# Kernel optimization log

Measured on AMD Instinct MI355X. Metric: run time of the kernel, lower is better.

Reference implementation:

```python
import jax, jax.numpy as jnp
import numpy as np

DIM = 384
HEADS = 6
HIDDEN = int(DIM * 4.0)
EPS = 1e-6

def setup_inputs() -> dict:
    key = jax.random.key(0)
    ks = jax.random.split(key, 8)
    s = 0.02
    return {
        "x": jax.random.normal(ks[0], (4, 2048, DIM), dtype=jnp.float32),
        "w_qkv": jax.random.normal(ks[1], (DIM, 3 * DIM), dtype=jnp.float32) * s,
        "b_qkv": jnp.zeros((3 * DIM,), dtype=jnp.float32),
        "w_proj": jax.random.normal(ks[2], (DIM, DIM), dtype=jnp.float32) * s,
        "b_proj": jnp.zeros((DIM,), dtype=jnp.float32),
        "w_fc1": jax.random.normal(ks[3], (DIM, HIDDEN), dtype=jnp.float32) * s,
        "b_fc1": jnp.zeros((HIDDEN,), dtype=jnp.float32),
        "w_fc2": jax.random.normal(ks[4], (HIDDEN, DIM), dtype=jnp.float32) * s,
        "b_fc2": jnp.zeros((DIM,), dtype=jnp.float32),
        "g1": jnp.ones((DIM,), dtype=jnp.float32),
        "beta1": jnp.zeros((DIM,), dtype=jnp.float32),
        "g2": jnp.ones((DIM,), dtype=jnp.float32),
        "beta2": jnp.zeros((DIM,), dtype=jnp.float32),
    }

def _layernorm(x, g, b):
    mu = jnp.mean(x, axis=-1, keepdims=True)
    var = jnp.mean(jnp.square(x - mu), axis=-1, keepdims=True)
    return (x - mu) * jax.lax.rsqrt(var + EPS) * g + b

def _attention(x, w_qkv, b_qkv, w_proj, b_proj):
    B, N, C = x.shape
    H = HEADS
    Dh = C // H
    qkv = x @ w_qkv + b_qkv                      # [B,N,3C]
    qkv = qkv.reshape(B, N, 3, H, Dh)
    q = jnp.transpose(qkv[:, :, 0], (0, 2, 1, 3))  # [B,H,N,Dh]
    k = jnp.transpose(qkv[:, :, 1], (0, 2, 1, 3))
    v = jnp.transpose(qkv[:, :, 2], (0, 2, 1, 3))
    scale = Dh ** -0.5
    attn = jnp.einsum('bhnd,bhmd->bhnm', q, k) * scale
    attn = jax.nn.softmax(attn, axis=-1)
    out = jnp.einsum('bhnm,bhmd->bhnd', attn, v)
    out = jnp.transpose(out, (0, 2, 1, 3)).reshape(B, N, C)
    return out @ w_proj + b_proj

def _mlp(x, w_fc1, b_fc1, w_fc2, b_fc2):
    h = jax.nn.gelu(x @ w_fc1 + b_fc1, approximate=False)
    return h @ w_fc2 + b_fc2

def reference(x, w_qkv, b_qkv, w_proj, b_proj, w_fc1, b_fc1, w_fc2, b_fc2, g1, beta1, g2, beta2):
    x = x + _attention(_layernorm(x, g1, beta1), w_qkv, b_qkv, w_proj, b_proj)
    x = x + _mlp(_layernorm(x, g2, beta2), w_fc1, b_fc1, w_fc2, b_fc2)
    return x
```

## Files before the change

kernel.cpp:

```cpp
#include <hip/hip_runtime.h>
#include <hip/hip_bf16.h>

#define TOK 8192
#define CDIM 384
#define HEADS 6
#define DH 64
#define HID 1536
#define SEQ 2048

#define QSCALE 0.18033688011112042f

typedef short bf16x8 __attribute__((ext_vector_type(8)));
typedef short bf16x4 __attribute__((ext_vector_type(4)));
typedef float f32x4 __attribute__((ext_vector_type(4)));
typedef void __attribute__((address_space(1))) GV;
typedef void __attribute__((address_space(3))) SV;

__device__ __forceinline__ short f2bf(float f) {
    __hip_bfloat16 h = __float2bfloat16(f);
    return *reinterpret_cast<short*>(&h);
}

__device__ __forceinline__ int pack_bf2(float a, float b) {
    __hip_bfloat162 h2 = __float22bfloat162_rn(make_float2(a, b));
    int r;
    __builtin_memcpy(&r, &h2, 4);
    return r;
}

__device__ __forceinline__ void gl_lds16(const short* g, short* lds) {
    __builtin_amdgcn_global_load_lds((GV*)g, (SV*)lds, 16, 0, 0);
}

__device__ __forceinline__ float gelu_exact(float v) {
    return 0.5f * v * (1.0f + erff(v * 0.70710678118654752f));
}

__global__ __launch_bounds__(128) void ln_kernel(const float* __restrict__ x,
                                                 const float* __restrict__ g,
                                                 const float* __restrict__ bta,
                                                 short* __restrict__ y) {
    const int row = blockIdx.x;
    const float* xr = x + (size_t)row * CDIM;
    const int t = threadIdx.x;
    float v0 = xr[t], v1 = xr[t + 128], v2 = xr[t + 256];
    float s = v0 + v1 + v2;
    float ss = v0 * v0 + v1 * v1 + v2 * v2;
#pragma unroll
    for (int off = 1; off < 64; off <<= 1) {
        s += __shfl_xor(s, off);
        ss += __shfl_xor(ss, off);
    }
    __shared__ float sh[4];
    const int wv = t >> 6;
    if ((t & 63) == 0) { sh[wv] = s; sh[2 + wv] = ss; }
    __syncthreads();
    s = sh[0] + sh[1];
    ss = sh[2] + sh[3];
    const float mu = s * (1.0f / CDIM);
    const float var = ss * (1.0f / CDIM) - mu * mu;
    const float rs = rsqrtf(var + 1e-6f);
    short* yr = y + (size_t)row * CDIM;
    yr[t]       = f2bf((v0 - mu) * rs * g[t]       + bta[t]);
    yr[t + 128] = f2bf((v1 - mu) * rs * g[t + 128] + bta[t + 128]);
    yr[t + 256] = f2bf((v2 - mu) * rs * g[t + 256] + bta[t + 256]);
}

__global__ __launch_bounds__(256) void transpose_all(const float* __restrict__ w_qkv,
                                                     const float* __restrict__ w_proj,
                                                     const float* __restrict__ w_fc1,
                                                     const float* __restrict__ w_fc2,
                                                     short* __restrict__ qkvT,
                                                     short* __restrict__ projT,
                                                     short* __restrict__ fc1T,
                                                     short* __restrict__ fc2T) {
    int b = blockIdx.x;
    const float* w; short* o; int K, N, nb;
    if (b < 432)       { w = w_qkv;  o = qkvT;  K = 384;  N = 1152; nb = 36; }
    else if (b < 576)  { b -= 432;  w = w_proj; o = projT; K = 384;  N = 384;  nb = 12; }
    else if (b < 1152) { b -= 576;  w = w_fc1;  o = fc1T;  K = 384;  N = 1536; nb = 48; }
    else               { b -= 1152; w = w_fc2;  o = fc2T;  K = 1536; N = 384;  nb = 12; }
    const int bx = (b % nb) * 32, by = (b / nb) * 32;
    __shared__ float t[32][33];
    const int tx = threadIdx.x & 31, ty = threadIdx.x >> 5;
#pragma unroll
    for (int i = 0; i < 4; ++i)
        t[ty + i * 8][tx] = w[(size_t)(by + ty + i * 8) * N + bx + tx];
    __syncthreads();
#pragma unroll
    for (int i = 0; i < 4; ++i)
        o[(size_t)(bx + ty + i * 8) * K + by + tx] = f2bf(t[tx][ty + i * 8]);
}

template <int MODE, int MT>
__global__ __launch_bounds__(256) void mfma_gemm(const short* __restrict__ A,
                                                 const short* __restrict__ WT,
                                                 const float* __restrict__ bias,
                                                 const float* __restrict__ resid,
                                                 float* __restrict__ outF,
                                                 short* __restrict__ outB,
                                                 short* __restrict__ qb,
                                                 short* __restrict__ kb,
                                                 short* __restrict__ vtb,
                                                 int M, int N, int K) {
    constexpr int BN = (MT == 4) ? 128 : 64;
    __shared__ __align__(16) short As[128 * 64];
    __shared__ __align__(16) short Bs[BN * 64];

    const int tid  = threadIdx.x;
    const int w    = tid >> 6;
    const int lane = tid & 63;
    const int quad = lane >> 4;
    const int n15  = lane & 15;
    const int wr   = (MT == 4) ? (w >> 1) : w;
    const int wc   = (MT == 4) ? (w & 1) : 0;
    const int m0   = blockIdx.y * 128;
    const int n0   = blockIdx.x * BN;
    const int swz  = n15 & 7;

    f32x4 acc[MT][4];
#pragma unroll
    for (int i = 0; i < MT; ++i)
#pragma unroll
        for (int j = 0; j < 4; ++j) {
            acc[i][j][0] = 0; acc[i][j][1] = 0; acc[i][j][2] = 0; acc[i][j][3] = 0;
        }

    for (int k0 = 0; k0 < K; k0 += 64) {
        __syncthreads();
#pragma unroll
        for (int i = 0; i < 4; ++i) {
            const int c = i * 256 + tid;
            const int r = c >> 3, p = c & 7;
            gl_lds16(A + (size_t)(m0 + r) * K + k0 + ((p ^ (r & 7)) * 8),
                     As + (i * 256 + w * 64) * 8);
        }
#pragma unroll
        for (int i = 0; i < BN / 32; ++i) {
            const int c = i * 256 + tid;
            const int r = c >> 3, p = c & 7;
            gl_lds16(WT + (size_t)(n0 + r) * K + k0 + ((p ^ (r & 7)) * 8),
                     Bs + (i * 256 + w * 64) * 8);
        }
        __syncthreads();

#pragma unroll
        for (int kk = 0; kk < 2; ++kk) {
            bf16x8 af[MT], bfr[4];
#pragma unroll
            for (int mt = 0; mt < MT; ++mt)
                af[mt] = *(const bf16x8*)&As[(wr * (MT * 16) + mt * 16 + n15) * 64 +
                                             (((kk * 4 + quad) ^ swz) * 8)];
#pragma unroll
            for (int nt = 0; nt < 4; ++nt)
                bfr[nt] = *(const bf16x8*)&Bs[(wc * 64 + nt * 16 + n15) * 64 +
                                              (((kk * 4 + quad) ^ swz) * 8)];
#pragma unroll
            for (int mt = 0; mt < MT; ++mt)
#pragma unroll
                for (int nt = 0; nt < 4; ++nt)
                    acc[mt][nt] = __builtin_amdgcn_mfma_f32_16x16x32_bf16(af[mt], bfr[nt], acc[mt][nt], 0, 0, 0);
        }
    }

#pragma unroll
    for (int nt = 0; nt < 4; ++nt) {
        const int col = n0 + wc * 64 + nt * 16 + n15;
        const float bv = bias[col];
        if constexpr (MODE == 2) {
            const int part = col / CDIM;
            const int rem  = col - part * CDIM;
            const int h    = rem >> 6;
            const int d    = rem & 63;
#pragma unroll
            for (int mt = 0; mt < MT; ++mt) {
                const int r0 = m0 + wr * (MT * 16) + mt * 16 + quad * 4;
                const int bi = r0 >> 11;
                const int n  = r0 & 2047;
                if (part == 2) {
                    short4 pkv;
                    pkv.x = f2bf(acc[mt][nt][0] + bv);
                    pkv.y = f2bf(acc[mt][nt][1] + bv);
                    pkv.z = f2bf(acc[mt][nt][2] + bv);
                    pkv.w = f2bf(acc[mt][nt][3] + bv);
                    *(short4*)&vtb[((size_t)(bi * HEADS + h) * DH + d) * SEQ + n] = pkv;
                } else {
                    short* dst = (part == 0 ? qb : kb) +
                                 ((size_t)(bi * HEADS + h) * SEQ + n) * DH + d;
#pragma unroll
                    for (int rr = 0; rr < 4; ++rr) {
                        float o = acc[mt][nt][rr] + bv;
                        if (part == 0) o *= QSCALE;
                        dst[(size_t)rr * DH] = f2bf(o);
                    }
                }
            }
        } else {
#pragma unroll
            for (int mt = 0; mt < MT; ++mt)
#pragma unroll
                for (int rr = 0; rr < 4; ++rr) {
                    const int r = m0 + wr * (MT * 16) + mt * 16 + quad * 4 + rr;
                    float o = acc[mt][nt][rr] + bv;
                    if constexpr (MODE == 1) {
                        outB[(size_t)r * N + col] = f2bf(gelu_exact(o));
                    } else {
                        if (resid) o += resid[(size_t)r * N + col];
                        outF[(size_t)r * N + col] = o;
                    }
                }
        }
    }
}

__global__ __launch_bounds__(256) void attn_mfma(const short* __restrict__ qb,
                                                 const short* __restrict__ kb,
                                                 const short* __restrict__ vtb,
                                                 short* __restrict__ outp) {
    __shared__ __align__(16) short Ql[64 * 64];
    __shared__ __align__(16) short Kl[64 * 64];
    __shared__ __align__(16) short Vtl[64 * 64];

    const int qt = blockIdx.x;
    const int bh = blockIdx.z * HEADS + blockIdx.y;

    const int tid  = threadIdx.x;
    const int w    = tid >> 6;
    const int lane = tid & 63;
    const int quad = lane >> 4;
    const int n15  = lane & 15;
    const int swz  = n15 & 7;

    const size_t headoff = (size_t)bh * SEQ * DH;

    {
        const short* qg = qb + headoff + (size_t)qt * 64 * DH;
#pragma unroll
        for (int i = 0; i < 2; ++i) {
            const int c = (w * 2 + i) * 64 + lane;
            const int r = c >> 3, p = c & 7;
            gl_lds16(qg + r * 64 + ((p ^ (r & 7)) * 8), Ql + (c - lane) * 8);
        }
    }

    const short* kptr[2];
    const short* vptr[2];
#pragma unroll
    for (int i = 0; i < 2; ++i) {
        const int c = (w * 2 + i) * 64 + lane;
        const int r = c >> 3, p = c & 7;
        kptr[i] = kb + headoff + r * 64 + ((p ^ (r & 7)) * 8);
        vptr[i] = vtb + (size_t)bh * DH * SEQ + (size_t)r * SEQ + ((p ^ (r & 7)) * 8);
    }

    f32x4 O[4];
    float lacc = 0.0f;
#pragma unroll
    for (int nt = 0; nt < 4; ++nt) { O[nt][0] = 0; O[nt][1] = 0; O[nt][2] = 0; O[nt][3] = 0; }

    bf16x8 qf[2];

    for (int kt = 0; kt < SEQ / 64; ++kt) {
        __syncthreads();
#pragma unroll
        for (int i = 0; i < 2; ++i) {
            gl_lds16(kptr[i], Kl + ((w * 2 + i) * 64) * 8);
            gl_lds16(vptr[i], Vtl + ((w * 2 + i) * 64) * 8);
            kptr[i] += 64 * DH;
            vptr[i] += 64;
        }
        __syncthreads();

        if (kt == 0) {
            qf[0] = *(const bf16x8*)&Ql[(w * 16 + n15) * 64 + ((quad ^ swz) * 8)];
            qf[1] = *(const bf16x8*)&Ql[(w * 16 + n15) * 64 + (((4 + quad) ^ swz) * 8)];
        }

        f32x4 S[4];
#pragma unroll
        for (int nt = 0; nt < 4; ++nt) {
            S[nt][0] = 0; S[nt][1] = 0; S[nt][2] = 0; S[nt][3] = 0;
#pragma unroll
            for (int kc = 0; kc < 2; ++kc) {
                const bf16x8 kf = *(const bf16x8*)&Kl[(nt * 16 + n15) * 64 + (((kc * 4 + quad) ^ swz) * 8)];
                S[nt] = __builtin_amdgcn_mfma_f32_16x16x32_bf16(kf, qf[kc], S[nt], 0, 0, 0);
            }
        }

        bf16x4 af16[4];
#pragma unroll
        for (int nt = 0; nt < 4; ++nt) {
            float p0 = exp2f(S[nt][0]), p1 = exp2f(S[nt][1]);
            float p2 = exp2f(S[nt][2]), p3 = exp2f(S[nt][3]);
            lacc += (p0 + p1) + (p2 + p3);
            int pk[2];
            pk[0] = pack_bf2(p0, p1);
            pk[1] = pack_bf2(p2, p3);
            __builtin_memcpy(&af16[nt], pk, 8);
        }

#pragma unroll
        for (int kc16 = 0; kc16 < 4; ++kc16) {
#pragma unroll
            for (int ntd = 0; ntd < 4; ++ntd) {
                const int row = ntd * 16 + n15;
                const int pchunk = (2 * kc16 + (quad >> 1)) ^ swz;
                const bf16x4 vf = *(const bf16x4*)&Vtl[row * 64 + pchunk * 8 + (quad & 1) * 4];
                O[ntd] = __builtin_amdgcn_mfma_f32_16x16x16bf16_1k(af16[kc16], vf, O[ntd], 0, 0, 0);
            }
        }
    }

    lacc += __shfl_xor(lacc, 16);
    lacc += __shfl_xor(lacc, 32);
    const float invq = 1.0f / lacc;
#pragma unroll
    for (int rr = 0; rr < 4; ++rr) {
        const float inv = __shfl(invq, quad * 4 + rr);
        const int row = qt * 64 + w * 16 + quad * 4 + rr;
#pragma unroll
        for (int nt = 0; nt < 4; ++nt)
            outp[(size_t)(blockIdx.z * SEQ + row) * CDIM + blockIdx.y * DH + nt * 16 + n15] =
                f2bf(O[nt][rr] * inv);
    }
}

extern "C" void kernel_launch(void* const* d_in, const int* in_sizes, int n_in,
                              void* d_out, int out_size, void* d_ws, size_t ws_size,
                              hipStream_t stream) {
    const float* x      = (const float*)d_in[0];
    const float* w_qkv  = (const float*)d_in[1];
    const float* b_qkv  = (const float*)d_in[2];
    const float* w_proj = (const float*)d_in[3];
    const float* b_proj = (const float*)d_in[4];
    const float* w_fc1  = (const float*)d_in[5];
    const float* b_fc1  = (const float*)d_in[6];
    const float* w_fc2  = (const float*)d_in[7];
    const float* b_fc2  = (const float*)d_in[8];
    const float* g1     = (const float*)d_in[9];
    const float* beta1  = (const float*)d_in[10];
    const float* g2     = (const float*)d_in[11];
    const float* beta2  = (const float*)d_in[12];
    float* out = (float*)d_out;

    short* qkvT = (short*)d_ws;
    short* projT = qkvT + 1152 * 384;
    short* fc1T  = projT + 384 * 384;
    short* fc2T  = fc1T + 1536 * 384;
    short* y     = fc2T + 384 * 1536;
    short* qb    = y + (size_t)TOK * 384;
    short* kb    = qb + (size_t)TOK * 384;
    short* vtb   = kb + (size_t)TOK * 384;
    short* attn  = vtb + (size_t)TOK * 384;
    short* hbuf  = attn + (size_t)TOK * 384;

    transpose_all<<<1728, 256, 0, stream>>>(w_qkv, w_proj, w_fc1, w_fc2,
                                            qkvT, projT, fc1T, fc2T);

    ln_kernel<<<TOK, 128, 0, stream>>>(x, g1, beta1, y);
    mfma_gemm<2, 4><<<dim3(1152 / 128, TOK / 128), 256, 0, stream>>>(
        y, qkvT, b_qkv, nullptr, nullptr, nullptr, qb, kb, vtb, TOK, 3 * CDIM, CDIM);
    attn_mfma<<<dim3(SEQ / 64, HEADS, 4), 256, 0, stream>>>(qb, kb, vtb, attn);
    mfma_gemm<0, 2><<<dim3(CDIM / 64, TOK / 128), 256, 0, stream>>>(
        attn, projT, b_proj, x, out, nullptr, nullptr, nullptr, nullptr, TOK, CDIM, CDIM);
    ln_kernel<<<TOK, 128, 0, stream>>>(out, g2, beta2, y);
    mfma_gemm<1, 4><<<dim3(HID / 128, TOK / 128), 256, 0, stream>>>(
        y, fc1T, b_fc1, nullptr, nullptr, hbuf, nullptr, nullptr, nullptr, TOK, HID, CDIM);
    mfma_gemm<0, 2><<<dim3(CDIM / 64, TOK / 128), 256, 0, stream>>>(
        hbuf, fc2T, b_fc2, out, out, nullptr, nullptr, nullptr, nullptr, TOK, CDIM, HID);
}
```

Baseline: 255.5 us.

## Double-buffer attention K/V, fuse LN with weight transpose, shrink GEMM tiles

Attention now double-buffers the K and V^T tiles in LDS, prefetching the next tile while the current one is computed, so one barrier per iteration is removed. It also computes the softmax row sums with an extra MFMA against a ones vector instead of scalar adds and shuffles. The first layernorm and the weight transpose are merged into one launch, and the N=384 projection and fc2 GEMMs switch to 64-row tiles to put more blocks on the GPU. The trade-offs are double the LDS use in attention, denominators summed from bf16-rounded probabilities, and less data reuse per GEMM block.

Result: faster. 244.8 us (-4.2%).

```diff
diff --git a/kernel.cpp b/kernel.cpp
--- a/kernel.cpp
+++ b/kernel.cpp
@@ -34,6 +34,63 @@
 
 __device__ __forceinline__ float gelu_exact(float v) {
     return 0.5f * v * (1.0f + erff(v * 0.70710678118654752f));
+}
+
+__global__ __launch_bounds__(128) void ln_trans(const float* __restrict__ x,
+                                                const float* __restrict__ g,
+                                                const float* __restrict__ bta,
+                                                short* __restrict__ y,
+                                                const float* __restrict__ w_qkv,
+                                                const float* __restrict__ w_proj,
+                                                const float* __restrict__ w_fc1,
+                                                const float* __restrict__ w_fc2,
+                                                short* __restrict__ qkvT,
+                                                short* __restrict__ projT,
+                                                short* __restrict__ fc1T,
+                                                short* __restrict__ fc2T) {
+    if (blockIdx.x < TOK) {
+        const int row = blockIdx.x;
+        const float* xr = x + (size_t)row * CDIM;
+        const int t = threadIdx.x;
+        float v0 = xr[t], v1 = xr[t + 128], v2 = xr[t + 256];
+        float s = v0 + v1 + v2;
+        float ss = v0 * v0 + v1 * v1 + v2 * v2;
+#pragma unroll
+        for (int off = 1; off < 64; off <<= 1) {
+            s += __shfl_xor(s, off);
+            ss += __shfl_xor(ss, off);
+        }
+        __shared__ float sh[4];
+        const int wv = t >> 6;
+        if ((t & 63) == 0) { sh[wv] = s; sh[2 + wv] = ss; }
+        __syncthreads();
+        s = sh[0] + sh[1];
+        ss = sh[2] + sh[3];
+        const float mu = s * (1.0f / CDIM);
+        const float var = ss * (1.0f / CDIM) - mu * mu;
+        const float rs = rsqrtf(var + 1e-6f);
+        short* yr = y + (size_t)row * CDIM;
+        yr[t]       = f2bf((v0 - mu) * rs * g[t]       + bta[t]);
+        yr[t + 128] = f2bf((v1 - mu) * rs * g[t + 128] + bta[t + 128]);
+        yr[t + 256] = f2bf((v2 - mu) * rs * g[t + 256] + bta[t + 256]);
+        return;
+    }
+    int b = blockIdx.x - TOK;
+    const float* w; short* o; int K, N, nb;
+    if (b < 432)       { w = w_qkv;  o = qkvT;  K = 384;  N = 1152; nb = 36; }
+    else if (b < 576)  { b -= 432;  w = w_proj; o = projT; K = 384;  N = 384;  nb = 12; }
+    else if (b < 1152) { b -= 576;  w = w_fc1;  o = fc1T;  K = 384;  N = 1536; nb = 48; }
+    else               { b -= 1152; w = w_fc2;  o = fc2T;  K = 1536; N = 384;  nb = 12; }
+    const int bx = (b % nb) * 32, by = (b / nb) * 32;
+    __shared__ float t[32][33];
+    const int tx = threadIdx.x & 31, ty = threadIdx.x >> 5;
+#pragma unroll
+    for (int i = 0; i < 8; ++i)
+        t[ty + i * 4][tx] = w[(size_t)(by + ty + i * 4) * N + bx + tx];
+    __syncthreads();
+#pragma unroll
+    for (int i = 0; i < 8; ++i)
+        o[(size_t)(bx + ty + i * 4) * K + by + tx] = f2bf(t[tx][ty + i * 4]);
 }
 
 __global__ __launch_bounds__(128) void ln_kernel(const float* __restrict__ x,
@@ -66,32 +123,6 @@
     yr[t + 256] = f2bf((v2 - mu) * rs * g[t + 256] + bta[t + 256]);
 }
 
-__global__ __launch_bounds__(256) void transpose_all(const float* __restrict__ w_qkv,
-                                                     const float* __restrict__ w_proj,
-                                                     const float* __restrict__ w_fc1,
-                                                     const float* __restrict__ w_fc2,
-                                                     short* __restrict__ qkvT,
-                                                     short* __restrict__ projT,
-                                                     short* __restrict__ fc1T,
-                                                     short* __restrict__ fc2T) {
-    int b = blockIdx.x;
-    const float* w; short* o; int K, N, nb;
-    if (b < 432)       { w = w_qkv;  o = qkvT;  K = 384;  N = 1152; nb = 36; }
-    else if (b < 576)  { b -= 432;  w = w_proj; o = projT; K = 384;  N = 384;  nb = 12; }
-    else if (b < 1152) { b -= 576;  w = w_fc1;  o = fc1T;  K = 384;  N = 1536; nb = 48; }
-    else               { b -= 1152; w = w_fc2;  o = fc2T;  K = 1536; N = 384;  nb = 12; }
-    const int bx = (b % nb) * 32, by = (b / nb) * 32;
-    __shared__ float t[32][33];
-    const int tx = threadIdx.x & 31, ty = threadIdx.x >> 5;
-#pragma unroll
-    for (int i = 0; i < 4; ++i)
-        t[ty + i * 8][tx] = w[(size_t)(by + ty + i * 8) * N + bx + tx];
-    __syncthreads();
-#pragma unroll
-    for (int i = 0; i < 4; ++i)
-        o[(size_t)(bx + ty + i * 8) * K + by + tx] = f2bf(t[tx][ty + i * 8]);
-}
-
 template <int MODE, int MT>
 __global__ __launch_bounds__(256) void mfma_gemm(const short* __restrict__ A,
                                                  const short* __restrict__ WT,
@@ -104,7 +135,8 @@
                                                  short* __restrict__ vtb,
                                                  int M, int N, int K) {
     constexpr int BN = (MT == 4) ? 128 : 64;
-    __shared__ __align__(16) short As[128 * 64];
+    constexpr int BM = (MT == 1) ? 64 : 128;
+    __shared__ __align__(16) short As[BM * 64];
     __shared__ __align__(16) short Bs[BN * 64];
 
     const int tid  = threadIdx.x;
@@ -114,7 +146,7 @@
     const int n15  = lane & 15;
     const int wr   = (MT == 4) ? (w >> 1) : w;
     const int wc   = (MT == 4) ? (w & 1) : 0;
-    const int m0   = blockIdx.y * 128;
+    const int m0   = blockIdx.y * BM;
     const int n0   = blockIdx.x * BN;
     const int swz  = n15 & 7;
 
@@ -129,7 +161,7 @@
     for (int k0 = 0; k0 < K; k0 += 64) {
         __syncthreads();
 #pragma unroll
-        for (int i = 0; i < 4; ++i) {
+        for (int i = 0; i < BM / 32; ++i) {
             const int c = i * 256 + tid;
             const int r = c >> 3, p = c & 7;
             gl_lds16(A + (size_t)(m0 + r) * K + k0 + ((p ^ (r & 7)) * 8),
@@ -218,8 +250,8 @@
                                                  const short* __restrict__ vtb,
                                                  short* __restrict__ outp) {
     __shared__ __align__(16) short Ql[64 * 64];
-    __shared__ __align__(16) short Kl[64 * 64];
-    __shared__ __align__(16) short Vtl[64 * 64];
+    __shared__ __align__(16) short Kl[2][64 * 64];
+    __shared__ __align__(16) short Vtl[2][64 * 64];
 
     const int qt = blockIdx.x;
     const int bh = blockIdx.z * HEADS + blockIdx.y;
@@ -253,23 +285,37 @@
         vptr[i] = vtb + (size_t)bh * DH * SEQ + (size_t)r * SEQ + ((p ^ (r & 7)) * 8);
     }
 
-    f32x4 O[4];
-    float lacc = 0.0f;
+#pragma unroll
+    for (int i = 0; i < 2; ++i) {
+        gl_lds16(kptr[i], Kl[0] + ((w * 2 + i) * 64) * 8);
+        gl_lds16(vptr[i], Vtl[0] + ((w * 2 + i) * 64) * 8);
+        kptr[i] += 64 * DH;
+        vptr[i] += 64;
+    }
+
+    f32x4 O[4], O4;
+    O4[0] = 0; O4[1] = 0; O4[2] = 0; O4[3] = 0;
 #pragma unroll
     for (int nt = 0; nt < 4; ++nt) { O[nt][0] = 0; O[nt][1] = 0; O[nt][2] = 0; O[nt][3] = 0; }
 
+    bf16x4 onesf;
+    { const short one = 0x3F80; onesf[0] = one; onesf[1] = one; onesf[2] = one; onesf[3] = one; }
+
     bf16x8 qf[2];
 
     for (int kt = 0; kt < SEQ / 64; ++kt) {
+        const int cur = kt & 1;
         __syncthreads();
-#pragma unroll
-        for (int i = 0; i < 2; ++i) {
-            gl_lds16(kptr[i], Kl + ((w * 2 + i) * 64) * 8);
-            gl_lds16(vptr[i], Vtl + ((w * 2 + i) * 64) * 8);
-            kptr[i] += 64 * DH;
-            vptr[i] += 64;
-        }
-        __syncthreads();
+        if (kt < SEQ / 64 - 1) {
+            const int nxt = cur ^ 1;
+#pragma unroll
+            for (int i = 0; i < 2; ++i) {
+                gl_lds16(kptr[i], Kl[nxt] + ((w * 2 + i) * 64) * 8);
+                gl_lds16(vptr[i], Vtl[nxt] + ((w * 2 + i) * 64) * 8);
+                kptr[i] += 64 * DH;
+                vptr[i] += 64;
+            }
+        }
 
         if (kt == 0) {
             qf[0] = *(const bf16x8*)&Ql[(w * 16 + n15) * 64 + ((quad ^ swz) * 8)];
@@ -282,7 +328,7 @@
             S[nt][0] = 0; S[nt][1] = 0; S[nt][2] = 0; S[nt][3] = 0;
 #pragma unroll
             for (int kc = 0; kc < 2; ++kc) {
-                const bf16x8 kf = *(const bf16x8*)&Kl[(nt * 16 + n15) * 64 + (((kc * 4 + quad) ^ swz) * 8)];
+                const bf16x8 kf = *(const bf16x8*)&Kl[cur][(nt * 16 + n15) * 64 + (((kc * 4 + quad) ^ swz) * 8)];
                 S[nt] = __builtin_amdgcn_mfma_f32_16x16x32_bf16(kf, qf[kc], S[nt], 0, 0, 0);
             }
         }
@@ -290,12 +336,9 @@
         bf16x4 af16[4];
 #pragma unroll
         for (int nt = 0; nt < 4; ++nt) {
-            float p0 = exp2f(S[nt][0]), p1 = exp2f(S[nt][1]);
-            float p2 = exp2f(S[nt][2]), p3 = exp2f(S[nt][3]);
-            lacc += (p0 + p1) + (p2 + p3);
             int pk[2];
-            pk[0] = pack_bf2(p0, p1);
-            pk[1] = pack_bf2(p2, p3);
+            pk[0] = pack_bf2(exp2f(S[nt][0]), exp2f(S[nt][1]));
+            pk[1] = pack_bf2(exp2f(S[nt][2]), exp2f(S[nt][3]));
             __builtin_memcpy(&af16[nt], pk, 8);
         }
 
@@ -305,18 +348,16 @@
             for (int ntd = 0; ntd < 4; ++ntd) {
                 const int row = ntd * 16 + n15;
                 const int pchunk = (2 * kc16 + (quad >> 1)) ^ swz;
-                const bf16x4 vf = *(const bf16x4*)&Vtl[row * 64 + pchunk * 8 + (quad & 1) * 4];
+                const bf16x4 vf = *(const bf16x4*)&Vtl[cur][row * 64 + pchunk * 8 + (quad & 1) * 4];
                 O[ntd] = __builtin_amdgcn_mfma_f32_16x16x16bf16_1k(af16[kc16], vf, O[ntd], 0, 0, 0);
             }
-        }
-    }
-
-    lacc += __shfl_xor(lacc, 16);
-    lacc += __shfl_xor(lacc, 32);
-    const float invq = 1.0f / lacc;
+            O4 = __builtin_amdgcn_mfma_f32_16x16x16bf16_1k(af16[kc16], onesf, O4, 0, 0, 0);
+        }
+    }
+
 #pragma unroll
     for (int rr = 0; rr < 4; ++rr) {
-        const float inv = __shfl(invq, quad * 4 + rr);
+        const float inv = 1.0f / O4[rr];
         const int row = qt * 64 + w * 16 + quad * 4 + rr;
 #pragma unroll
         for (int nt = 0; nt < 4; ++nt)
@@ -354,18 +395,17 @@
     short* attn  = vtb + (size_t)TOK * 384;
     short* hbuf  = attn + (size_t)TOK * 384;
 
-    transpose_all<<<1728, 256, 0, stream>>>(w_qkv, w_proj, w_fc1, w_fc2,
-                                            qkvT, projT, fc1T, fc2T);
-
-    ln_kernel<<<TOK, 128, 0, stream>>>(x, g1, beta1, y);
+    ln_trans<<<TOK + 1728, 128, 0, stream>>>(x, g1, beta1, y,
+                                             w_qkv, w_proj, w_fc1, w_fc2,
+                                             qkvT, projT, fc1T, fc2T);
     mfma_gemm<2, 4><<<dim3(1152 / 128, TOK / 128), 256, 0, stream>>>(
         y, qkvT, b_qkv, nullptr, nullptr, nullptr, qb, kb, vtb, TOK, 3 * CDIM, CDIM);
     attn_mfma<<<dim3(SEQ / 64, HEADS, 4), 256, 0, stream>>>(qb, kb, vtb, attn);
-    mfma_gemm<0, 2><<<dim3(CDIM / 64, TOK / 128), 256, 0, stream>>>(
+    mfma_gemm<0, 1><<<dim3(CDIM / 64, TOK / 64), 256, 0, stream>>>(
         attn, projT, b_proj, x, out, nullptr, nullptr, nullptr, nullptr, TOK, CDIM, CDIM);
     ln_kernel<<<TOK, 128, 0, stream>>>(out, g2, beta2, y);
     mfma_gemm<1, 4><<<dim3(HID / 128, TOK / 128), 256, 0, stream>>>(
         y, fc1T, b_fc1, nullptr, nullptr, hbuf, nullptr, nullptr, nullptr, TOK, HID, CDIM);
-    mfma_gemm<0, 2><<<dim3(CDIM / 64, TOK / 128), 256, 0, stream>>>(
+    mfma_gemm<0, 1><<<dim3(CDIM / 64, TOK / 64), 256, 0, stream>>>(
         hbuf, fc2T, b_fc2, out, out, nullptr, nullptr, nullptr, nullptr, TOK, CDIM, HID);
 }
```
